# Kernel optimization log

Hardware: AMD Instinct MI355X
Metric: run time of the kernel (lower is better)

The kernel has to match this reference:

```python
import jax, jax.numpy as jnp
import numpy as np

H, DK = 8, 32
D_MODEL = H * DK  # 256
Q_DIM = K_DIM = V_DIM = 256
B, T, S = 4, 4, 1024
NEG = -1e10


def setup_inputs() -> dict:
    rng = jax.random.key(0)
    ks = jax.random.split(rng, 12)
    w = lambda k, shp: (jax.random.normal(k, shp, jnp.float32) * 0.02)
    return {
        "query": jax.random.normal(ks[0], (B, T, S, Q_DIM), jnp.float32),
        "key": jax.random.normal(ks[1], (B, T, S, K_DIM), jnp.float32),
        "value": jax.random.normal(ks[2], (B, T, S, V_DIM), jnp.float32),
        "mask": jax.random.randint(ks[3], (B, T), 1, S + 1),  # valid lengths in [1, S]
        "Wq": w(ks[4], (D_MODEL, Q_DIM)), "bq": jnp.zeros((D_MODEL,), jnp.float32),
        "Wk": w(ks[5], (D_MODEL, K_DIM)), "bk": jnp.zeros((D_MODEL,), jnp.float32),
        "Wv": w(ks[6], (D_MODEL, V_DIM)), "bv": jnp.zeros((D_MODEL,), jnp.float32),
        "Wo": w(ks[7], (Q_DIM, D_MODEL)), "bo": jnp.zeros((Q_DIM,), jnp.float32),
    }


def reference(query, key, value, mask, Wq, bq, Wk, bk, Wv, bv, Wo, bo):
    b, t, s, _ = query.shape
    # projections -> [B,T,h,S,d_k]
    def proj(x, W, bias):
        y = jnp.einsum('btsf,df->btsd', x, W) + bias
        return y.reshape(b, t, s, H, DK).transpose(0, 1, 3, 2, 4)
    q = proj(query, Wq, bq)
    k = proj(key, Wk, bk)
    v = proj(value, Wv, bv)
    # scores [B,T,h,S,S]
    scores = jnp.einsum('bthqd,bthkd->bthqk', q, k) / jnp.sqrt(jnp.float32(DK))
    # vectorized length mask: positions < len on both axes (replaces torch python loop)
    valid = jnp.arange(s)[None, None, :] < mask[:, :, None]        # [B,T,S]
    m = valid[:, :, None, :, None] & valid[:, :, None, None, :]    # [B,T,1,S,S]
    scores = jnp.where(m, scores, NEG)
    p = jax.nn.softmax(scores, axis=-1)
    x = jnp.einsum('bthqk,bthkd->bthqd', p, v)                     # [B,T,h,S,d_k]
    x = x.transpose(0, 1, 3, 2, 4).reshape(b, t, s, H * DK)
    return jnp.einsum('btsd,qd->btsq', x, Wo) + bo
```

## Files before the change

kernel.cpp:

```cpp
#include <hip/hip_runtime.h>

#define EXPC 0.25505654442163f

typedef __attribute__((ext_vector_type(8))) short bfrag;
typedef __attribute__((ext_vector_type(4))) float ffrag;
typedef __attribute__((ext_vector_type(8))) unsigned int u8v;
typedef __attribute__((ext_vector_type(4))) unsigned int u4v;
typedef __attribute__((ext_vector_type(2))) unsigned int u2v;

__device__ __forceinline__ short f2bf(float x) {
  union { float f; unsigned u; } v; v.f = x;
  return (short)((v.u + 0x8000u) >> 16);
}

__device__ __forceinline__ float bf2f(short s) {
  union { float f; unsigned u; } v;
  v.u = ((unsigned)(unsigned short)s) << 16;
  return v.f;
}

__device__ __forceinline__ unsigned int packbf(float a, float b) {
  return __builtin_amdgcn_perm(__float_as_uint(b) + 0x8000u,
                               __float_as_uint(a) + 0x8000u, 0x07060302u);
}

__device__ __forceinline__ bfrag cvtp(u8v x) {
  u4v r;
#pragma unroll
  for (int i = 0; i < 4; ++i)
    r[i] = __builtin_amdgcn_perm(x[2 * i + 1] + 0x8000u, x[2 * i] + 0x8000u, 0x07060302u);
  union { u4v u; bfrag b; } c; c.u = r; return c.b;
}

__global__ __launch_bounds__(256, 4) void proj_kv(
    const float* __restrict__ kin, const float* __restrict__ Wk,
    const float* __restrict__ bk, const float* __restrict__ vin,
    const float* __restrict__ Wv, const float* __restrict__ bv,
    short* __restrict__ ko, short* __restrict__ vt) {
  const int t = threadIdx.x;
  const int lane = t & 63, wid = t >> 6;
  const int lrow = lane & 15, lq = lane >> 4;
  __shared__ __align__(16) char lds[18432];
  const int row4 = t >> 2, c4 = (t & 3) * 8;

  const bool isK = blockIdx.x < 512;
  if (isK) {
    const int bx = blockIdx.x >> 1, d0 = (blockIdx.x & 1) * 128;
    const int m0 = bx * 64;
    short* Ab = (short*)lds;
    short* Bb = (short*)(lds + 5120);
    short* tile = (short*)lds;
    ffrag acc[4][2] = {};
    u8v pa, pb0, pb1;
    pa  = *(const u8v*)(kin + (size_t)(m0 + row4) * 256 + c4);
    pb0 = *(const u8v*)(Wk + (size_t)(d0 + row4) * 256 + c4);
    pb1 = *(const u8v*)(Wk + (size_t)(d0 + 64 + row4) * 256 + c4);
    *(bfrag*)(Ab + row4 * 40 + c4) = cvtp(pa);
    *(bfrag*)(Bb + row4 * 40 + c4) = cvtp(pb0);
    *(bfrag*)(Bb + (64 + row4) * 40 + c4) = cvtp(pb1);
#pragma unroll 1
    for (int s = 0; s < 8; ++s) {
      __syncthreads();
      if (s < 7) {
        const int k1 = (s + 1) * 32;
        pa  = *(const u8v*)(kin + (size_t)(m0 + row4) * 256 + k1 + c4);
        pb0 = *(const u8v*)(Wk + (size_t)(d0 + row4) * 256 + k1 + c4);
        pb1 = *(const u8v*)(Wk + (size_t)(d0 + 64 + row4) * 256 + k1 + c4);
      }
      bfrag a[4], b[2];
#pragma unroll
      for (int i = 0; i < 4; ++i)
        a[i] = *(const bfrag*)(Ab + (i * 16 + lrow) * 40 + lq * 8);
#pragma unroll
      for (int j = 0; j < 2; ++j)
        b[j] = *(const bfrag*)(Bb + (wid * 32 + j * 16 + lrow) * 40 + lq * 8);
#pragma unroll
      for (int i = 0; i < 4; ++i)
#pragma unroll
        for (int j = 0; j < 2; ++j)
          acc[i][j] = __builtin_amdgcn_mfma_f32_16x16x32_bf16(a[i], b[j], acc[i][j], 0, 0, 0);
      __syncthreads();
      if (s < 7) {
        *(bfrag*)(Ab + row4 * 40 + c4) = cvtp(pa);
        *(bfrag*)(Bb + row4 * 40 + c4) = cvtp(pb0);
        *(bfrag*)(Bb + (64 + row4) * 40 + c4) = cvtp(pb1);
      }
    }
    __syncthreads();
#pragma unroll
    for (int j = 0; j < 2; ++j) {
      int dl = wid * 32 + j * 16 + lrow;
      float bs = bk[d0 + dl];
#pragma unroll
      for (int i = 0; i < 4; ++i)
#pragma unroll
        for (int r = 0; r < 4; ++r)
          tile[(i * 16 + lq * 4 + r) * 136 + dl] = f2bf(acc[i][j][r] + bs);
    }
    __syncthreads();
#pragma unroll
    for (int p = 0; p < 4; ++p) {
      int id2 = p * 256 + t;
      int row = id2 >> 4, c = id2 & 15;
      bfrag v = *(const bfrag*)(tile + row * 136 + c * 8);
      *(bfrag*)(ko + (size_t)(m0 + row) * 256 + d0 + c * 8) = v;
    }
  } else {
    const int t2 = blockIdx.x - 512;
    const int bx = t2 >> 1, d0 = (t2 & 1) * 128;
    const int n0 = bx * 64;
    short* Aw = (short*)lds;
    short* Bv = (short*)(lds + 10240);
    short* tile = (short*)lds;
    ffrag acc[2][4] = {};
    u8v pv, pw0, pw1;
    pw0 = *(const u8v*)(Wv + (size_t)(d0 + row4) * 256 + c4);
    pw1 = *(const u8v*)(Wv + (size_t)(d0 + 64 + row4) * 256 + c4);
    pv  = *(const u8v*)(vin + (size_t)(n0 + row4) * 256 + c4);
    *(bfrag*)(Aw + row4 * 40 + c4) = cvtp(pw0);
    *(bfrag*)(Aw + (64 + row4) * 40 + c4) = cvtp(pw1);
    *(bfrag*)(Bv + row4 * 40 + c4) = cvtp(pv);
#pragma unroll 1
    for (int s = 0; s < 8; ++s) {
      __syncthreads();
      if (s < 7) {
        const int k1 = (s + 1) * 32;
        pw0 = *(const u8v*)(Wv + (size_t)(d0 + row4) * 256 + k1 + c4);
        pw1 = *(const u8v*)(Wv + (size_t)(d0 + 64 + row4) * 256 + k1 + c4);
        pv  = *(const u8v*)(vin + (size_t)(n0 + row4) * 256 + k1 + c4);
      }
      bfrag a[2], b[4];
#pragma unroll
      for (int i = 0; i < 2; ++i)
        a[i] = *(const bfrag*)(Aw + (wid * 32 + i * 16 + lrow) * 40 + lq * 8);
#pragma unroll
      for (int j = 0; j < 4; ++j)
        b[j] = *(const bfrag*)(Bv + (j * 16 + lrow) * 40 + lq * 8);
#pragma unroll
      for (int i = 0; i < 2; ++i)
#pragma unroll
        for (int j = 0; j < 4; ++j)
          acc[i][j] = __builtin_amdgcn_mfma_f32_16x16x32_bf16(a[i], b[j], acc[i][j], 0, 0, 0);
      __syncthreads();
      if (s < 7) {
        *(bfrag*)(Aw + row4 * 40 + c4) = cvtp(pw0);
        *(bfrag*)(Aw + (64 + row4) * 40 + c4) = cvtp(pw1);
        *(bfrag*)(Bv + row4 * 40 + c4) = cvtp(pv);
      }
    }
    __syncthreads();
#pragma unroll
    for (int i = 0; i < 2; ++i)
#pragma unroll
      for (int r = 0; r < 4; ++r) {
        int dl = wid * 32 + i * 16 + lq * 4 + r;
        float bs = bv[d0 + dl];
#pragma unroll
        for (int j = 0; j < 4; ++j)
          tile[dl * 72 + j * 16 + lrow] = f2bf(acc[i][j][r] + bs);
      }
    __syncthreads();
    const int bt = n0 >> 10, sl0 = n0 & 1023;
#pragma unroll
    for (int p = 0; p < 4; ++p) {
      int id2 = p * 256 + t;
      int dl = id2 >> 3, c = id2 & 7;
      bfrag v = *(const bfrag*)(tile + dl * 72 + c * 8);
      *(bfrag*)(vt + (size_t)bt * 262144 + (size_t)(d0 + dl) * 1024 + sl0 + c * 8) = v;
    }
  }
}

__global__ __launch_bounds__(256, 4) void attn_half(
    const float* __restrict__ query, const float* __restrict__ Wq,
    const float* __restrict__ bq, const float* __restrict__ Wo,
    const float* __restrict__ bo, const short* __restrict__ K,
    const short* __restrict__ Vt, const int* __restrict__ mask,
    float* __restrict__ out) {
  const int lane = threadIdx.x & 63, wid = threadIdx.x >> 6;
  const int lrow = lane & 15, lq = lane >> 4;
  const int id = blockIdx.x;
  const int hb = id & 1;
  const int bt = (((id >> 1) & 15) + (id >> 9)) & 15;
  const int qt = id >> 5;
  const int q0 = qt * 32;
  const int L = mask[bt];
  const int h = hb * 4 + wid;
  const int nvalid = min(max(L - q0, 0), 32);
  if (nvalid <= 0) return;

  __shared__ __align__(16) short qx[32 * 136];
  __shared__ __align__(16) unsigned int ptbuf[4][16 * 36];
  unsigned int* ptg = &ptbuf[wid][0];

  const short* Vb = Vt + ((size_t)bt * 8 + h) * 32768;
  float l_i[2];
  ffrag o[2][2] = {};

  {
    const int n0 = h * 32;
    const float* X = query + ((size_t)bt * 1024 + q0) * 256;
    ffrag acc[2][2] = {};
    u8v xa[2], wb[2], xa_n[2], wb_n[2];
#pragma unroll
    for (int i = 0; i < 2; ++i)
      xa[i] = *(const u8v*)(X + (size_t)(i * 16 + lrow) * 256 + lq * 8);
#pragma unroll
    for (int j = 0; j < 2; ++j)
      wb[j] = *(const u8v*)(Wq + (size_t)(n0 + j * 16 + lrow) * 256 + lq * 8);
#pragma unroll 1
    for (int tt = 0; tt < 8; ++tt) {
      if (tt < 7) {
        const int kk = (tt + 1) * 32;
#pragma unroll
        for (int i = 0; i < 2; ++i)
          xa_n[i] = *(const u8v*)(X + (size_t)(i * 16 + lrow) * 256 + kk + lq * 8);
#pragma unroll
        for (int j = 0; j < 2; ++j)
          wb_n[j] = *(const u8v*)(Wq + (size_t)(n0 + j * 16 + lrow) * 256 + kk + lq * 8);
      }
      bfrag a[2], b[2];
#pragma unroll
      for (int i = 0; i < 2; ++i) a[i] = cvtp(xa[i]);
#pragma unroll
      for (int j = 0; j < 2; ++j) b[j] = cvtp(wb[j]);
#pragma unroll
      for (int i = 0; i < 2; ++i)
#pragma unroll
        for (int j = 0; j < 2; ++j)
          acc[i][j] = __builtin_amdgcn_mfma_f32_16x16x32_bf16(a[i], b[j], acc[i][j], 0, 0, 0);
#pragma unroll
      for (int i = 0; i < 2; ++i) xa[i] = xa_n[i];
#pragma unroll
      for (int j = 0; j < 2; ++j) wb[j] = wb_n[j];
    }
#pragma unroll
    for (int j = 0; j < 2; ++j) {
      float bs = bq[n0 + j * 16 + lrow];
#pragma unroll
      for (int i = 0; i < 2; ++i)
#pragma unroll
        for (int r = 0; r < 4; ++r)
          qx[(i * 16 + lq * 4 + r) * 136 + wid * 32 + j * 16 + lrow] =
              f2bf((acc[i][j][r] + bs) * EXPC);
    }
  }

  {
    const short* Kb = K + (size_t)bt * 262144;
    bfrag qf[2];
#pragma unroll
    for (int g = 0; g < 2; ++g)
      qf[g] = *(const bfrag*)(qx + (g * 16 + lrow) * 136 + wid * 32 + lq * 8);

    const int nchunk = (L + 63) >> 6;
    float l_loc[2] = {0.f, 0.f};
    bfrag kf[4], kf_n[4];
#pragma unroll
    for (int f = 0; f < 4; ++f)
      kf[f] = *(const bfrag*)(Kb + (size_t)(f * 16 + lrow) * 256 + h * 32 + lq * 8);

#pragma unroll 1
    for (int c = 0; c < nchunk; ++c) {
      const int kc = c * 64;
      const ffrag zf = {0.f, 0.f, 0.f, 0.f};
      if (c + 1 < nchunk) {
#pragma unroll
        for (int f = 0; f < 4; ++f)
          kf_n[f] = *(const bfrag*)(Kb + (size_t)(kc + 64 + f * 16 + lrow) * 256 + h * 32 + lq * 8);
      }
      bfrag av[2][2];
#pragma unroll
      for (int dj = 0; dj < 2; ++dj)
#pragma unroll
        for (int b = 0; b < 2; ++b)
          av[dj][b] = *(const bfrag*)(Vb + (size_t)(dj * 16 + lrow) * 1024 + kc + b * 32 + lq * 8);

      ffrag st[2][4];
#pragma unroll
      for (int g = 0; g < 2; ++g)
#pragma unroll
        for (int f = 0; f < 4; ++f)
          st[g][f] = __builtin_amdgcn_mfma_f32_16x16x32_bf16(kf[f], qf[g], zf, 0, 0, 0);

      const bool fullc = (kc + 64 <= L);
#pragma unroll
      for (int g = 0; g < 2; ++g) {
        float p[4][4];
        if (fullc) {
#pragma unroll
          for (int f = 0; f < 4; ++f)
#pragma unroll
            for (int r = 0; r < 4; ++r) {
              p[f][r] = __builtin_amdgcn_exp2f(st[g][f][r]);
              l_loc[g] += p[f][r];
            }
        } else {
#pragma unroll
          for (int f = 0; f < 4; ++f)
#pragma unroll
            for (int r = 0; r < 4; ++r) {
              int kr = kc + f * 16 + lq * 4 + r;
              float pv = (kr < L) ? __builtin_amdgcn_exp2f(st[g][f][r]) : 0.f;
              p[f][r] = pv;
              l_loc[g] += pv;
            }
        }
#pragma unroll
        for (int f = 0; f < 4; ++f) {
          u2v w;
          w[0] = packbf(p[f][0], p[f][1]);
          w[1] = packbf(p[f][2], p[f][3]);
          *(u2v*)(ptg + lrow * 36 + 8 * f + 2 * lq) = w;
        }
#pragma unroll
        for (int b = 0; b < 2; ++b) {
          u4v pv = *(const u4v*)(ptg + lrow * 36 + 16 * b + 4 * lq);
          union { u4v u; bfrag bf; } pt; pt.u = pv;
#pragma unroll
          for (int dj = 0; dj < 2; ++dj)
            o[g][dj] = __builtin_amdgcn_mfma_f32_16x16x32_bf16(av[dj][b], pt.bf, o[g][dj], 0, 0, 0);
        }
      }
#pragma unroll
      for (int f = 0; f < 4; ++f) kf[f] = kf_n[f];
    }

#pragma unroll
    for (int g = 0; g < 2; ++g) {
      float rs = l_loc[g];
      rs += __shfl_xor(rs, 16);
      rs += __shfl_xor(rs, 32);
      l_i[g] = rs;
    }
  }

#pragma unroll
  for (int g = 0; g < 2; ++g) {
    float rcp = 1.0f / l_i[g];
#pragma unroll
    for (int dj = 0; dj < 2; ++dj) {
      u2v w;
      w[0] = packbf(o[g][dj][0] * rcp, o[g][dj][1] * rcp);
      w[1] = packbf(o[g][dj][2] * rcp, o[g][dj][3] * rcp);
      *(u2v*)(qx + (g * 16 + lrow) * 136 + wid * 32 + dj * 16 + lq * 4) = w;
    }
  }
  __syncthreads();

  {
    const int n0p = wid * 64;
    ffrag acc[2][4] = {};
#pragma unroll 1
    for (int tt = 0; tt < 4; ++tt) {
      const int k0 = tt * 32;
      bfrag a0 = *(const bfrag*)(qx + lrow * 136 + k0 + lq * 8);
      bfrag a1 = *(const bfrag*)(qx + (16 + lrow) * 136 + k0 + lq * 8);
#pragma unroll
      for (int j = 0; j < 4; ++j) {
        bfrag b = cvtp(*(const u8v*)(Wo + (size_t)(n0p + j * 16 + lrow) * 256 + hb * 128 + k0 + lq * 8));
        acc[0][j] = __builtin_amdgcn_mfma_f32_16x16x32_bf16(a0, b, acc[0][j], 0, 0, 0);
        acc[1][j] = __builtin_amdgcn_mfma_f32_16x16x32_bf16(a1, b, acc[1][j], 0, 0, 0);
      }
    }
#pragma unroll
    for (int j = 0; j < 4; ++j) {
      const int dcol = n0p + j * 16 + lrow;
      const float bs = hb ? 0.f : bo[dcol];
#pragma unroll
      for (int i = 0; i < 2; ++i)
#pragma unroll
        for (int r = 0; r < 4; ++r) {
          int qr = q0 + i * 16 + lq * 4 + r;
          if (qr < L)
            atomicAdd(out + ((size_t)bt * 1024 + qr) * 256 + dcol, acc[i][j][r] + bs);
        }
    }
  }
}

__global__ __launch_bounds__(256, 2) void bcast_fill(
    const short* __restrict__ Vt, const float* __restrict__ Wo,
    const float* __restrict__ bo, const int* __restrict__ mask,
    float* __restrict__ out) {
  const int bt = blockIdx.x;
  const int L = mask[bt];
  const int d = threadIdx.x;
  __shared__ float xm[256];
  {
    const int hh = d >> 5, dl = d & 31;
    const short* vr = Vt + ((size_t)bt * 8 + hh) * 32768 + dl * 1024;
    float s = 0.f;
#pragma unroll 4
    for (int i = 0; i < 1024; i += 8) {
      bfrag v = *(const bfrag*)(vr + i);
#pragma unroll
      for (int j = 0; j < 8; ++j) s += bf2f(v[j]);
    }
    xm[d] = s * (1.0f / 1024.0f);
  }
  __syncthreads();
  float acc = bo[d];
  const float* wr = Wo + (size_t)d * 256;
#pragma unroll 4
  for (int k = 0; k < 256; k += 4) {
    float4 w4 = *(const float4*)(wr + k);
    acc += xm[k] * w4.x + xm[k + 1] * w4.y + xm[k + 2] * w4.z + xm[k + 3] * w4.w;
  }
  float* ob = out + (size_t)bt * 1024 * 256 + d;
#pragma unroll 1
  for (int row = L; row < 1024; ++row)
    ob[(size_t)row * 256] = acc;
}

extern "C" void kernel_launch(void* const* d_in, const int* in_sizes, int n_in,
                              void* d_out, int out_size, void* d_ws, size_t ws_size,
                              hipStream_t stream) {
  const float* query = (const float*)d_in[0];
  const float* key   = (const float*)d_in[1];
  const float* value = (const float*)d_in[2];
  const int*   mask  = (const int*)d_in[3];
  const float* Wq = (const float*)d_in[4];
  const float* bq = (const float*)d_in[5];
  const float* Wk = (const float*)d_in[6];
  const float* bk = (const float*)d_in[7];
  const float* Wv = (const float*)d_in[8];
  const float* bv = (const float*)d_in[9];
  const float* Wo = (const float*)d_in[10];
  const float* bo = (const float*)d_in[11];
  float* out = (float*)d_out;

  short* k_ws  = (short*)d_ws;
  short* vt_ws = k_ws + 4194304;

  proj_kv<<<dim3(1024), 256, 0, stream>>>(key, Wk, bk, value, Wv, bv, k_ws, vt_ws);
  attn_half<<<dim3(1024), 256, 0, stream>>>(query, Wq, bq, Wo, bo,
                                            k_ws, vt_ws, mask, out);
  bcast_fill<<<dim3(16), 256, 0, stream>>>(vt_ws, Wo, bo, mask, out);
}
```

Measured before the change: 250.7 us.

## Fuse head halves into one 1024-thread block with split-key attention reduction

The attention kernel now runs all 8 heads for a 32-query tile in one 16-wave block instead of two 4-head blocks. Each head's key range is split across two waves whose partial outputs and row sums are combined through shared memory. Because one block now owns the full output projection, it writes the output with plain stores instead of atomicAdd and no longer needs per-head-half partial sums. The cost is larger blocks, extra block-wide barriers and a shared-memory reduction step, and fewer resident blocks per CU.

```diff
diff --git a/kernel.cpp b/kernel.cpp
--- a/kernel.cpp
+++ b/kernel.cpp
@@ -171,7 +171,7 @@
   }
 }
 
-__global__ __launch_bounds__(256, 4) void attn_half(
+__global__ __launch_bounds__(1024, 8) void attn_fused(
     const float* __restrict__ query, const float* __restrict__ Wq,
     const float* __restrict__ bq, const float* __restrict__ Wo,
     const float* __restrict__ bo, const short* __restrict__ K,
@@ -179,32 +179,30 @@
     float* __restrict__ out) {
   const int lane = threadIdx.x & 63, wid = threadIdx.x >> 6;
   const int lrow = lane & 15, lq = lane >> 4;
+  const int h = wid & 7, s = wid >> 3;
   const int id = blockIdx.x;
-  const int hb = id & 1;
-  const int bt = (((id >> 1) & 15) + (id >> 9)) & 15;
-  const int qt = id >> 5;
+  const int bt = (id + (id >> 8)) & 15;
+  const int qt = id >> 4;
   const int q0 = qt * 32;
   const int L = mask[bt];
-  const int h = hb * 4 + wid;
   const int nvalid = min(max(L - q0, 0), 32);
   if (nvalid <= 0) return;
 
-  __shared__ __align__(16) short qx[32 * 136];
-  __shared__ __align__(16) unsigned int ptbuf[4][16 * 36];
+  __shared__ __align__(16) short qx[32 * 264];
+  __shared__ __align__(16) unsigned int ptbuf[16][16 * 36];
   unsigned int* ptg = &ptbuf[wid][0];
 
   const short* Vb = Vt + ((size_t)bt * 8 + h) * 32768;
   float l_i[2];
+  float l_loc[2] = {0.f, 0.f};
   ffrag o[2][2] = {};
 
   {
     const int n0 = h * 32;
-    const float* X = query + ((size_t)bt * 1024 + q0) * 256;
-    ffrag acc[2][2] = {};
-    u8v xa[2], wb[2], xa_n[2], wb_n[2];
-#pragma unroll
-    for (int i = 0; i < 2; ++i)
-      xa[i] = *(const u8v*)(X + (size_t)(i * 16 + lrow) * 256 + lq * 8);
+    const float* X = query + ((size_t)bt * 1024 + q0 + s * 16) * 256;
+    ffrag acc[2] = {};
+    u8v xa, wb[2], xa_n, wb_n[2];
+    xa = *(const u8v*)(X + (size_t)lrow * 256 + lq * 8);
 #pragma unroll
     for (int j = 0; j < 2; ++j)
       wb[j] = *(const u8v*)(Wq + (size_t)(n0 + j * 16 + lrow) * 256 + lq * 8);
@@ -212,25 +210,18 @@
     for (int tt = 0; tt < 8; ++tt) {
       if (tt < 7) {
         const int kk = (tt + 1) * 32;
-#pragma unroll
-        for (int i = 0; i < 2; ++i)
-          xa_n[i] = *(const u8v*)(X + (size_t)(i * 16 + lrow) * 256 + kk + lq * 8);
+        xa_n = *(const u8v*)(X + (size_t)lrow * 256 + kk + lq * 8);
 #pragma unroll
         for (int j = 0; j < 2; ++j)
           wb_n[j] = *(const u8v*)(Wq + (size_t)(n0 + j * 16 + lrow) * 256 + kk + lq * 8);
       }
-      bfrag a[2], b[2];
-#pragma unroll
-      for (int i = 0; i < 2; ++i) a[i] = cvtp(xa[i]);
-#pragma unroll
-      for (int j = 0; j < 2; ++j) b[j] = cvtp(wb[j]);
-#pragma unroll
-      for (int i = 0; i < 2; ++i)
-#pragma unroll
-        for (int j = 0; j < 2; ++j)
-          acc[i][j] = __builtin_amdgcn_mfma_f32_16x16x32_bf16(a[i], b[j], acc[i][j], 0, 0, 0);
-#pragma unroll
-      for (int i = 0; i < 2; ++i) xa[i] = xa_n[i];
+      bfrag a = cvtp(xa);
+#pragma unroll
+      for (int j = 0; j < 2; ++j) {
+        bfrag b = cvtp(wb[j]);
+        acc[j] = __builtin_amdgcn_mfma_f32_16x16x32_bf16(a, b, acc[j], 0, 0, 0);
+      }
+      xa = xa_n;
 #pragma unroll
       for (int j = 0; j < 2; ++j) wb[j] = wb_n[j];
     }
@@ -238,33 +229,37 @@
     for (int j = 0; j < 2; ++j) {
       float bs = bq[n0 + j * 16 + lrow];
 #pragma unroll
-      for (int i = 0; i < 2; ++i)
-#pragma unroll
-        for (int r = 0; r < 4; ++r)
-          qx[(i * 16 + lq * 4 + r) * 136 + wid * 32 + j * 16 + lrow] =
-              f2bf((acc[i][j][r] + bs) * EXPC);
-    }
-  }
+      for (int r = 0; r < 4; ++r)
+        qx[(s * 16 + lq * 4 + r) * 264 + n0 + j * 16 + lrow] =
+            f2bf((acc[j][r] + bs) * EXPC);
+    }
+  }
+  __syncthreads();
 
   {
     const short* Kb = K + (size_t)bt * 262144;
     bfrag qf[2];
 #pragma unroll
     for (int g = 0; g < 2; ++g)
-      qf[g] = *(const bfrag*)(qx + (g * 16 + lrow) * 136 + wid * 32 + lq * 8);
+      qf[g] = *(const bfrag*)(qx + (g * 16 + lrow) * 264 + h * 32 + lq * 8);
 
     const int nchunk = (L + 63) >> 6;
-    float l_loc[2] = {0.f, 0.f};
+    const int nc0 = (nchunk + 1) >> 1;
+    const int cbeg = s ? nc0 : 0;
+    const int cend = s ? nchunk : nc0;
+
     bfrag kf[4], kf_n[4];
-#pragma unroll
-    for (int f = 0; f < 4; ++f)
-      kf[f] = *(const bfrag*)(Kb + (size_t)(f * 16 + lrow) * 256 + h * 32 + lq * 8);
-
-#pragma unroll 1
-    for (int c = 0; c < nchunk; ++c) {
+    if (cbeg < cend) {
+#pragma unroll
+      for (int f = 0; f < 4; ++f)
+        kf[f] = *(const bfrag*)(Kb + (size_t)(cbeg * 64 + f * 16 + lrow) * 256 + h * 32 + lq * 8);
+    }
+
+#pragma unroll 1
+    for (int c = cbeg; c < cend; ++c) {
       const int kc = c * 64;
       const ffrag zf = {0.f, 0.f, 0.f, 0.f};
-      if (c + 1 < nchunk) {
+      if (c + 1 < cend) {
 #pragma unroll
         for (int f = 0; f < 4; ++f)
           kf_n[f] = *(const bfrag*)(Kb + (size_t)(kc + 64 + f * 16 + lrow) * 256 + h * 32 + lq * 8);
@@ -325,7 +320,32 @@
 #pragma unroll
       for (int f = 0; f < 4; ++f) kf[f] = kf_n[f];
     }
-
+  }
+
+  __syncthreads();
+  float* cb = (float*)&ptbuf[0][0];
+  if (s == 1) {
+    float* dst = cb + ((size_t)(h * 64 + lane)) * 18;
+#pragma unroll
+    for (int g = 0; g < 2; ++g)
+#pragma unroll
+      for (int dj = 0; dj < 2; ++dj)
+#pragma unroll
+        for (int r = 0; r < 4; ++r) dst[g * 8 + dj * 4 + r] = o[g][dj][r];
+    dst[16] = l_loc[0];
+    dst[17] = l_loc[1];
+  }
+  __syncthreads();
+  if (s == 0) {
+    const float* src = cb + ((size_t)(h * 64 + lane)) * 18;
+#pragma unroll
+    for (int g = 0; g < 2; ++g)
+#pragma unroll
+      for (int dj = 0; dj < 2; ++dj)
+#pragma unroll
+        for (int r = 0; r < 4; ++r) o[g][dj][r] += src[g * 8 + dj * 4 + r];
+    l_loc[0] += src[16];
+    l_loc[1] += src[17];
 #pragma unroll
     for (int g = 0; g < 2; ++g) {
       float rs = l_loc[g];
@@ -333,49 +353,46 @@
       rs += __shfl_xor(rs, 32);
       l_i[g] = rs;
     }
-  }
-
-#pragma unroll
-  for (int g = 0; g < 2; ++g) {
-    float rcp = 1.0f / l_i[g];
-#pragma unroll
-    for (int dj = 0; dj < 2; ++dj) {
-      u2v w;
-      w[0] = packbf(o[g][dj][0] * rcp, o[g][dj][1] * rcp);
-      w[1] = packbf(o[g][dj][2] * rcp, o[g][dj][3] * rcp);
-      *(u2v*)(qx + (g * 16 + lrow) * 136 + wid * 32 + dj * 16 + lq * 4) = w;
+#pragma unroll
+    for (int g = 0; g < 2; ++g) {
+      float rcp = 1.0f / l_i[g];
+#pragma unroll
+      for (int dj = 0; dj < 2; ++dj) {
+        u2v w;
+        w[0] = packbf(o[g][dj][0] * rcp, o[g][dj][1] * rcp);
+        w[1] = packbf(o[g][dj][2] * rcp, o[g][dj][3] * rcp);
+        *(u2v*)(qx + (g * 16 + lrow) * 264 + h * 32 + dj * 16 + lq * 4) = w;
+      }
     }
   }
   __syncthreads();
 
   {
-    const int n0p = wid * 64;
-    ffrag acc[2][4] = {};
-#pragma unroll 1
-    for (int tt = 0; tt < 4; ++tt) {
-      const int k0 = tt * 32;
-      bfrag a0 = *(const bfrag*)(qx + lrow * 136 + k0 + lq * 8);
-      bfrag a1 = *(const bfrag*)(qx + (16 + lrow) * 136 + k0 + lq * 8);
-#pragma unroll
-      for (int j = 0; j < 4; ++j) {
-        bfrag b = cvtp(*(const u8v*)(Wo + (size_t)(n0p + j * 16 + lrow) * 256 + hb * 128 + k0 + lq * 8));
-        acc[0][j] = __builtin_amdgcn_mfma_f32_16x16x32_bf16(a0, b, acc[0][j], 0, 0, 0);
-        acc[1][j] = __builtin_amdgcn_mfma_f32_16x16x32_bf16(a1, b, acc[1][j], 0, 0, 0);
-      }
-    }
-#pragma unroll
-    for (int j = 0; j < 4; ++j) {
-      const int dcol = n0p + j * 16 + lrow;
-      const float bs = hb ? 0.f : bo[dcol];
-#pragma unroll
-      for (int i = 0; i < 2; ++i)
-#pragma unroll
-        for (int r = 0; r < 4; ++r) {
-          int qr = q0 + i * 16 + lq * 4 + r;
-          if (qr < L)
-            atomicAdd(out + ((size_t)bt * 1024 + qr) * 256 + dcol, acc[i][j][r] + bs);
-        }
-    }
+    const int n0p = wid * 16;
+    ffrag acc[2] = {};
+    u8v wv = *(const u8v*)(Wo + (size_t)(n0p + lrow) * 256 + lq * 8);
+    u8v wv_n;
+#pragma unroll 1
+    for (int tt = 0; tt < 8; ++tt) {
+      if (tt < 7)
+        wv_n = *(const u8v*)(Wo + (size_t)(n0p + lrow) * 256 + (tt + 1) * 32 + lq * 8);
+      bfrag b = cvtp(wv);
+      bfrag a0 = *(const bfrag*)(qx + lrow * 264 + tt * 32 + lq * 8);
+      bfrag a1 = *(const bfrag*)(qx + (16 + lrow) * 264 + tt * 32 + lq * 8);
+      acc[0] = __builtin_amdgcn_mfma_f32_16x16x32_bf16(a0, b, acc[0], 0, 0, 0);
+      acc[1] = __builtin_amdgcn_mfma_f32_16x16x32_bf16(a1, b, acc[1], 0, 0, 0);
+      wv = wv_n;
+    }
+    const int d = n0p + lrow;
+    const float bs = bo[d];
+#pragma unroll
+    for (int i = 0; i < 2; ++i)
+#pragma unroll
+      for (int r = 0; r < 4; ++r) {
+        int qr = q0 + i * 16 + lq * 4 + r;
+        if (qr < L)
+          out[((size_t)bt * 1024 + qr) * 256 + d] = acc[i][r] + bs;
+      }
   }
 }
 
@@ -434,7 +451,7 @@
   short* vt_ws = k_ws + 4194304;
 
   proj_kv<<<dim3(1024), 256, 0, stream>>>(key, Wk, bk, value, Wv, bv, k_ws, vt_ws);
-  attn_half<<<dim3(1024), 256, 0, stream>>>(query, Wq, bq, Wo, bo,
-                                            k_ws, vt_ws, mask, out);
+  attn_fused<<<dim3(512), 1024, 0, stream>>>(query, Wq, bq, Wo, bo,
+                                             k_ws, vt_ws, mask, out);
   bcast_fill<<<dim3(16), 256, 0, stream>>>(vt_ws, Wo, bo, mask, out);
 }
```

Result: slower. 395.8 us (+57.9%).
